# Kernel optimization log

Measured on AMD Instinct MI355X. Metric: run time of the kernel, lower is better.

The kernel has to match this reference:

```python
import jax, jax.numpy as jnp
import numpy as np

B, D, K = 4194304, 32, 16
SCALE = 0.999  # the one-hot is filled with 0.999, not 1.0


def setup_inputs() -> dict:
    key = jax.random.key(0)
    k1, k2, k3 = jax.random.split(key, 3)
    attr_index = 5
    z = jax.random.normal(k1, (B, D), dtype=jnp.float32)
    # column attr_index holds integer shape-counter indices stored as floats
    idx = jax.random.randint(k2, (B,), 0, K)
    z = z.at[:, attr_index].set(idx.astype(jnp.float32))
    a = jax.random.uniform(k3, (B, K), dtype=jnp.float32)
    return {"z": z, "a": a, "attr_index": attr_index}


def reference(z, a, attr_index):
    # tensor_index = z[:, attr_index].long(); out[i] = 0.999 * a[i, tensor_index[i]]
    idx = z[:, attr_index].astype(jnp.int32)            # [B]
    gathered = jnp.take_along_axis(a, idx[:, None], axis=1)[:, 0]  # [B]
    return gathered * SCALE
```

## Files before the change

kernel.cpp:

```cpp
#include <hip/hip_runtime.h>
#include <hip/hip_bf16.h>


#define D_DIM 32
#define K_DIM 16
#define SCALE 0.999f

__global__ __launch_bounds__(256) void gather_valuation_kernel(
    const float* __restrict__ z,
    const float* __restrict__ a,
    const int* __restrict__ attr_p,
    float* __restrict__ out,
    int B)
{
    const int attr = attr_p[0];
    int i = blockIdx.x * blockDim.x + threadIdx.x;
    const int stride = gridDim.x * blockDim.x;
    for (; i < B; i += stride) {
        const int idx = (int)z[i * D_DIM + attr];
        out[i] = a[i * K_DIM + idx] * SCALE;
    }
}

extern "C" void kernel_launch(void* const* d_in, const int* in_sizes, int n_in,
                              void* d_out, int out_size, void* d_ws, size_t ws_size,
                              hipStream_t stream)
{
    const float* z    = (const float*)d_in[0];
    const float* a    = (const float*)d_in[1];
    const int*   attr = (const int*)d_in[2];
    float*       out  = (float*)d_out;

    const int B = out_size;

    const int block = 256;
    const int grid  = 2048;

    gather_valuation_kernel<<<grid, block, 0, stream>>>(z, a, attr, out, B);
}
```

Baseline: 150.1 us.

## Process four rows per thread with vectorized row loads and select-based gather

Each thread now handles four consecutive rows. It loads the whole 16-float row of `a` as four float4 vectors and picks the needed element with branch-free selects, instead of doing a data-dependent scalar gather. Results are written with one float4 store, and the grid is sized to cover B exactly rather than using a fixed grid-stride loop. The aim is more memory requests in flight per thread and wider, coalesced accesses. The cost is reading every element of `a` explicitly, plus an implicit assumption that B is a multiple of four with no tail handling.

```diff
diff --git a/kernel.cpp b/kernel.cpp
--- a/kernel.cpp
+++ b/kernel.cpp
@@ -5,6 +5,7 @@
 #define D_DIM 32
 #define K_DIM 16
 #define SCALE 0.999f
+#define ROWS  4
 
 __global__ __launch_bounds__(256) void gather_valuation_kernel(
     const float* __restrict__ z,
@@ -14,12 +15,36 @@
     int B)
 {
     const int attr = attr_p[0];
-    int i = blockIdx.x * blockDim.x + threadIdx.x;
-    const int stride = gridDim.x * blockDim.x;
-    for (; i < B; i += stride) {
-        const int idx = (int)z[i * D_DIM + attr];
-        out[i] = a[i * K_DIM + idx] * SCALE;
+    const long t    = (long)blockIdx.x * blockDim.x + threadIdx.x;
+    const long base = t * ROWS;
+    if (base >= B) return;
+
+    float zv[ROWS];
+#pragma unroll
+    for (int j = 0; j < ROWS; ++j)
+        zv[j] = z[(base + j) * D_DIM + attr];
+
+    const float4* __restrict__ a4 = (const float4*)a;
+    float4 q[ROWS][4];
+#pragma unroll
+    for (int j = 0; j < ROWS; ++j) {
+#pragma unroll
+        for (int c = 0; c < 4; ++c)
+            q[j][c] = a4[(base + j) * (K_DIM / 4) + c];
     }
+
+    float4 res;
+#pragma unroll
+    for (int j = 0; j < ROWS; ++j) {
+        const int idx = (int)zv[j];
+        const float4 qa = (idx & 8) ? ((idx & 4) ? q[j][3] : q[j][2])
+                                    : ((idx & 4) ? q[j][1] : q[j][0]);
+        const float  x  = (idx & 2) ? ((idx & 1) ? qa.w : qa.z)
+                                    : ((idx & 1) ? qa.y : qa.x);
+        ((float*)&res)[j] = x * SCALE;
+    }
+
+    *(float4*)(out + base) = res;
 }
 
 extern "C" void kernel_launch(void* const* d_in, const int* in_sizes, int n_in,
@@ -34,7 +59,7 @@
     const int B = out_size;
 
     const int block = 256;
-    const int grid  = 2048;
+    const int grid  = (B + block * ROWS - 1) / (block * ROWS);
 
     gather_valuation_kernel<<<grid, block, 0, stream>>>(z, a, attr, out, B);
 }
```

Measured after the change: 228.4 us. 1.52x slower.
